# Performance work log

Measured on AMD Instinct MI355X. Metric: run time of the kernel, lower is better.

The kernel has to match this reference:

```python
import jax, jax.numpy as jnp
import numpy as np

MODES = (16, 16)
EMBED_DIM = 64
NUM_HEADS = 8


def spectral_conv(x, w):
    """FNO-style spectral conv. x: [B,S,Ci,H,W]; w: [Ci,Co,mx,my,2] (real/imag)."""
    wc = w[..., 0] + 1j * w[..., 1]
    H, W = x.shape[-2], x.shape[-1]
    mx, my = wc.shape[2], wc.shape[3]
    xf = jnp.fft.rfft2(x)                                   # [B,S,Ci,H,W//2+1]
    of = jnp.einsum('bsixy,ioxy->bsoxy', xf[..., :mx, :my], wc)
    out_f = jnp.zeros(x.shape[:2] + (wc.shape[1], H, W // 2 + 1), dtype=of.dtype)
    out_f = out_f.at[..., :mx, :my].set(of)
    return jnp.fft.irfft2(out_f, s=(H, W))


def log_cpb_bias(n_sub_x, n_sub_y, w1, b1, w2):
    """Swin-v2-style log-spaced continuous position bias -> [heads, S, S]."""
    cx = jnp.arange(n_sub_x, dtype=jnp.float32)
    cy = jnp.arange(n_sub_y, dtype=jnp.float32)
    coords = jnp.stack(jnp.meshgrid(cx, cy, indexing='ij'), axis=-1).reshape(-1, 2)
    rel = coords[:, None, :] - coords[None, :, :]           # [S,S,2]
    rel = jnp.sign(rel) * jnp.log1p(jnp.abs(rel))
    h = jax.nn.relu(rel @ w1 + b1)                          # [S,S,hidden]
    bias = h @ w2                                           # [S,S,heads]
    return jnp.transpose(bias, (2, 0, 1))


def _unflatten(f, num_heads, embed_dim):
    # [B,S,h*d,H,W] -> [B,h,S,d,H,W]
    B, S = f.shape[0], f.shape[1]
    f = f.reshape(B, S, num_heads, embed_dim, f.shape[-2], f.shape[-1])
    return jnp.transpose(f, (0, 2, 1, 3, 4, 5))


def setup_inputs() -> dict:
    key = jax.random.key(0)
    ks = jax.random.split(key, 9)
    B, S, D, H, W = 2, 64, EMBED_DIM, 32, 32
    hd = NUM_HEADS * D
    mx, my = MODES
    scale = 0.02
    return {
        'seq': jax.random.normal(ks[0], (B, S, D, H, W), dtype=jnp.float32),
        'wq': scale * jax.random.normal(ks[1], (D, hd, mx, my, 2), dtype=jnp.float32),
        'wk': scale * jax.random.normal(ks[2], (D, hd, mx, my, 2), dtype=jnp.float32),
        'wv': scale * jax.random.normal(ks[3], (D, hd, mx, my, 2), dtype=jnp.float32),
        'wo': scale * jax.random.normal(ks[4], (hd, D, mx, my, 2), dtype=jnp.float32),
        'cpb_w1': scale * jax.random.normal(ks[5], (2, D), dtype=jnp.float32),
        'cpb_b1': jnp.zeros((D,), dtype=jnp.float32),
        'cpb_w2': scale * jax.random.normal(ks[6], (D, NUM_HEADS), dtype=jnp.float32),
        'n_sub_x': 8,
        'n_sub_y': 8,
    }


def reference(seq, wq, wk, wv, wo, cpb_w1, cpb_b1, cpb_w2, n_sub_x, n_sub_y):
    q = _unflatten(spectral_conv(seq, wq), NUM_HEADS, EMBED_DIM)  # [B,h,S,d,H,W]
    k = _unflatten(spectral_conv(seq, wk), NUM_HEADS, EMBED_DIM)
    v = _unflatten(spectral_conv(seq, wv), NUM_HEADS, EMBED_DIM)

    bias = log_cpb_bias(n_sub_x, n_sub_y, cpb_w1, cpb_b1, cpb_w2)  # [h,S,S]

    d, H, W = q.shape[-3], q.shape[-2], q.shape[-1]
    scale = 1.0 / jnp.sqrt(jnp.asarray(d * H * W, dtype=q.dtype))
    scores = jnp.einsum('bhqdxy,bhkdxy->bhqk', q, k) * scale + bias[None]
    attn = jax.nn.softmax(scores, axis=-1)
    sa = jnp.einsum('bhqk,bhkdxy->bhqdxy', attn, v)          # [B,h,S,d,H,W]

    # _flatten: [B,h,S,d,H,W] -> [B,S,h*d,H,W]
    sa = jnp.transpose(sa, (0, 2, 1, 3, 4, 5))
    B, S = sa.shape[0], sa.shape[1]
    sa = sa.reshape(B, S, NUM_HEADS * EMBED_DIM, H, W)
    return spectral_conv(sa, wo)
```

## Files before the change

kernel.cpp:

```cpp
#include <hip/hip_runtime.h>

#define TWO_PI 6.28318530717958647692f

#define NH 8
#define CH 128
#define NCH 2

#define OFF_XM   0ull
#define OFF_WTA  (OFF_XM + 8388608ull)
#define OFF_WTB  (OFF_WTA + 16777216ull)
#define OFF_PO   (OFF_WTB + 16777216ull)
#define OFF_ATTN (OFF_PO + 16777216ull)
#define WS_TOTAL (OFF_ATTN + 262144ull)

typedef short bf16x8 __attribute__((ext_vector_type(8)));
typedef float f32x4 __attribute__((ext_vector_type(4)));
#define MFMA_B16(a, b, c) __builtin_amdgcn_mfma_f32_16x16x32_bf16(a, b, c, 0, 0, 0)

__device__ __forceinline__ float bl(unsigned u) { return __uint_as_float(u << 16); }
__device__ __forceinline__ unsigned short f2b(float f) {
    unsigned u = __float_as_uint(f);
    return (unsigned short)((u + 0x7fffu + ((u >> 16) & 1u)) >> 16);
}
__device__ __forceinline__ unsigned pack2(float lo, float hi) {
    return (unsigned)f2b(lo) | ((unsigned)f2b(hi) << 16);
}

__device__ __forceinline__ bf16x8 mkfrag(const unsigned* __restrict__ Wt, int co_l, int ri,
                                         int ci0, bool dc) {
    unsigned a0 = Wt[(ci0 + 0) * 64 + (co_l ^ (ci0 + 0))];
    unsigned a1 = Wt[(ci0 + 1) * 64 + (co_l ^ (ci0 + 1))];
    unsigned a2 = Wt[(ci0 + 2) * 64 + (co_l ^ (ci0 + 2))];
    unsigned a3 = Wt[(ci0 + 3) * 64 + (co_l ^ (ci0 + 3))];
    uint4 r;
    if (ri) {
        if (dc) { r.x = 0u; r.y = 0u; r.z = 0u; r.w = 0u; }
        else {
            r.x = (a0 >> 16) | (a0 << 16); r.y = (a1 >> 16) | (a1 << 16);
            r.z = (a2 >> 16) | (a2 << 16); r.w = (a3 >> 16) | (a3 << 16);
        }
    } else {
        r.x = a0 ^ 0x80000000u; r.y = a1 ^ 0x80000000u;
        r.z = a2 ^ 0x80000000u; r.w = a3 ^ 0x80000000u;
    }
    return __builtin_bit_cast(bf16x8, r);
}

__global__ __launch_bounds__(256) void k_transpose2(const float* __restrict__ srcA, unsigned* __restrict__ dstA, int kindA,
                                                    const float* __restrict__ srcB, unsigned* __restrict__ dstB, int kindB,
                                                    int m0) {
    const float* in = (blockIdx.z == 0) ? srcA : srcB;
    unsigned* outp = (blockIdx.z == 0) ? dstA : dstB;
    int kind = (blockIdx.z == 0) ? kindA : kindB;
    __shared__ unsigned T[16][65];
    int tid = threadIdx.x;
    int r0 = blockIdx.x * 64;
    int ci, h;
    if (kind == 2) { h = r0 >> 12; ci = (r0 >> 6) & 63; }
    else           { ci = r0 >> 9; h = (r0 >> 6) & 7; }
    int ml0 = blockIdx.y * 16;
    int u = (m0 + ml0) >> 4;
    const float2* in2 = (const float2*)in;
    #pragma unroll
    for (int p = 0; p < 4; ++p) {
        int f = tid + p * 256;
        int row = f >> 4, mc = f & 15;
        float fac = (kind == 0) ? (mc > 0 ? 1.41421356f : (u > 0 ? 0.70710678f : 1.f))
                  : (kind == 1) ? (mc > 0 ? 1.f : (u > 0 ? 0.5f : 1.f)) : 1.f;
        float2 v = in2[(size_t)(r0 + row) * 256 + m0 + ml0 + mc];
        T[mc][row] = pack2(v.x * fac, v.y * fac);
    }
    __syncthreads();
    #pragma unroll
    for (int p = 0; p < 4; ++p) {
        int f = tid + p * 256;
        int ml = f >> 6, co = f & 63;
        outp[((size_t)((ml0 + ml) * 8 + h) << 12) + ci * 64 + co] = T[ml][co];
    }
}

__global__ __launch_bounds__(256) void k_rfft(const float* __restrict__ seq,
                                              unsigned short* __restrict__ XM) {
    __shared__ float c32[32], s32[32];
    __shared__ float fld[32][33];
    __shared__ float tre[512], tim[512];
    __shared__ float obuf[256][18];
    int tid = threadIdx.x;
    int cig = blockIdx.x;
    int bs = blockIdx.y;
    if (tid < 32) { float s, c; __sincosf(TWO_PI * tid / 32.0f, &s, &c); c32[tid] = c; s32[tid] = s; }
    for (int cl = 0; cl < 8; ++cl) {
        int ci = cig * 8 + cl;
        const float2* src = (const float2*)(seq + ((size_t)bs * 64 + ci) * 1024);
        for (int p = 0; p < 2; ++p) {
            int idx2 = tid + p * 256;
            float2 v = src[idx2];
            int x = idx2 >> 4, y2 = (idx2 & 15) * 2;
            fld[x][y2] = v.x; fld[x][y2 + 1] = v.y;
        }
        __syncthreads();
        for (int p = 0; p < 2; ++p) {
            int e = tid + p * 256;
            int x = e >> 4, v = e & 15;
            float sr = 0.f, si = 0.f;
            for (int y = 0; y < 32; ++y) {
                float f = fld[x][y];
                int ph = (v * y) & 31;
                sr = fmaf(f, c32[ph], sr);
                si = fmaf(-f, s32[ph], si);
            }
            tre[x * 16 + v] = sr; tim[x * 16 + v] = si;
        }
        __syncthreads();
        {
            int u = tid >> 4, v = tid & 15;
            float xr = 0.f, xi = 0.f;
            for (int x = 0; x < 32; ++x) {
                float tr = tre[x * 16 + v], ti = tim[x * 16 + v];
                int ph = (u * x) & 31;
                float c = c32[ph], s = s32[ph];
                xr += tr * c + ti * s;
                xi += ti * c - tr * s;
            }
            obuf[tid][cl * 2] = xr; obuf[tid][cl * 2 + 1] = xi;
        }
        __syncthreads();
    }
    uint4 a, b;
    a.x = pack2(obuf[tid][0], obuf[tid][1]);
    a.y = pack2(obuf[tid][2], obuf[tid][3]);
    a.z = pack2(obuf[tid][4], obuf[tid][5]);
    a.w = pack2(obuf[tid][6], obuf[tid][7]);
    b.x = pack2(obuf[tid][8], obuf[tid][9]);
    b.y = pack2(obuf[tid][10], obuf[tid][11]);
    b.z = pack2(obuf[tid][12], obuf[tid][13]);
    b.w = pack2(obuf[tid][14], obuf[tid][15]);
    uint4* op = (uint4*)(XM + (((size_t)tid * 128 + bs) * 64 + cig * 8) * 2);
    op[0] = a; op[1] = b;
}

__global__ __launch_bounds__(512) void k_qks(const unsigned short* __restrict__ XM,
                                             const unsigned* __restrict__ WQ,
                                             const unsigned* __restrict__ WK,
                                             float* __restrict__ part, int mbase) {
    __shared__ __align__(16) unsigned char Xs[16384];
    __shared__ __align__(16) unsigned Wq[4096];
    __shared__ __align__(16) unsigned Wk[4096];
    __shared__ __align__(16) unsigned char Qs[16384];
    __shared__ __align__(16) unsigned char Ks[16384];
    int tid = threadIdx.x;
    int mg = blockIdx.x, h = blockIdx.y, b = blockIdx.z;
    int lane = tid & 63, w = tid >> 6;
    int lr = lane & 15, lg = lane >> 4;
    int wr = w & 1, wc = w >> 1;
    int sxa = (lr & 7) << 4;
    int ri = lr & 1;
    f32x4 zf = {0.f, 0.f, 0.f, 0.f};
    f32x4 sacc[2];
    sacc[0] = zf; sacc[1] = zf;
    for (int mm = 0; mm < 4; ++mm) {
        int ml = mg * 4 + mm;
        int mode = mbase + ml;
        bool dc = (mode == 0);
        __syncthreads();
        {
            const unsigned short* xg = XM + ((size_t)mode * 128 + b * 64) * 128;
            #pragma unroll
            for (int p = 0; p < 2; ++p) {
                int g = tid + p * 512; int row = g >> 4, c16 = g & 15;
                uint4 v = *(const uint4*)(xg + row * 128 + c16 * 8);
                *(uint4*)(Xs + row * 256 + ((c16 * 16) ^ ((row & 7) << 4))) = v;
            }
        }
        {
            const unsigned* tq = WQ + ((size_t)(ml * 8 + h) << 12);
            const unsigned* tk = WK + ((size_t)(ml * 8 + h) << 12);
            #pragma unroll
            for (int p = 0; p < 16; ++p) {
                int idx = tid + p * 512;
                int r = idx & 4095;
                int ci = r >> 6, co = r & 63;
                if (idx < 4096) Wq[ci * 64 + (co ^ ci)] = tq[r];
                else            Wk[ci * 64 + (co ^ ci)] = tk[r];
            }
        }
        __syncthreads();
        {
            f32x4 qa[2][2], ka[2][2];
            #pragma unroll
            for (int m = 0; m < 2; ++m)
                #pragma unroll
                for (int n = 0; n < 2; ++n) { qa[m][n] = zf; ka[m][n] = zf; }
            #pragma unroll
            for (int ks = 0; ks < 4; ++ks) {
                int kb = (ks * 64 + lg * 16) ^ sxa;
                int ci0 = ks * 16 + lg * 4;
                bf16x8 a0 = *(const bf16x8*)(Xs + (wr * 32 + lr) * 256 + kb);
                bf16x8 a1 = *(const bf16x8*)(Xs + (wr * 32 + 16 + lr) * 256 + kb);
                #pragma unroll
                for (int n = 0; n < 2; ++n) {
                    int co_l = wc * 16 + n * 8 + (lr >> 1);
                    bf16x8 bq = mkfrag(Wq, co_l, ri, ci0, dc);
                    bf16x8 bk = mkfrag(Wk, co_l, ri, ci0, dc);
                    qa[0][n] = MFMA_B16(a0, bq, qa[0][n]);
                    qa[1][n] = MFMA_B16(a1, bq, qa[1][n]);
                    ka[0][n] = MFMA_B16(a0, bk, ka[0][n]);
                    ka[1][n] = MFMA_B16(a1, bk, ka[1][n]);
                }
            }
            #pragma unroll
            for (int m = 0; m < 2; ++m)
                #pragma unroll
                for (int n = 0; n < 2; ++n) {
                    int colb = (wc * 32 + n * 16 + lr) * 2;
                    #pragma unroll
                    for (int r = 0; r < 4; ++r) {
                        int row = wr * 32 + m * 16 + lg * 4 + r;
                        int swz = (row & 7) << 4;
                        *(unsigned short*)(Qs + row * 256 + (colb ^ swz)) = f2b(qa[m][n][r]);
                        *(unsigned short*)(Ks + row * 256 + (colb ^ swz)) = f2b(ka[m][n][r]);
                    }
                }
        }
        __syncthreads();
        {
            #pragma unroll
            for (int ks = 0; ks < 4; ++ks) {
                int kb = (ks * 64 + lg * 16) ^ sxa;
                bf16x8 a0 = *(const bf16x8*)(Qs + (wr * 32 + lr) * 256 + kb);
                bf16x8 a1 = *(const bf16x8*)(Qs + (wr * 32 + 16 + lr) * 256 + kb);
                bf16x8 b0 = *(const bf16x8*)(Ks + (wc * 16 + lr) * 256 + kb);
                sacc[0] = MFMA_B16(a0, b0, sacc[0]);
                sacc[1] = MFMA_B16(a1, b0, sacc[1]);
            }
        }
    }
    float* pp = part + (((size_t)((mbase >> 2) + mg) * 16 + b * 8 + h) << 12);
    #pragma unroll
    for (int m = 0; m < 2; ++m)
        #pragma unroll
        for (int r = 0; r < 4; ++r)
            pp[(wr * 32 + m * 16 + lg * 4 + r) * 64 + wc * 16 + lr] = sacc[m][r];
}

__global__ void k_softmax(const float* __restrict__ part,
                          const float* __restrict__ w1, const float* __restrict__ b1,
                          const float* __restrict__ w2, unsigned short* __restrict__ attnb) {
    int j = threadIdx.x;
    int i = blockIdx.x;
    int bh = blockIdx.y;
    int h = bh & 7;
    float s = 0.f;
    for (int mg = 0; mg < 64; ++mg)
        s += part[(((size_t)mg * 16 + bh) * 64 + i) * 64 + j];
    float dx = (float)((i >> 3) - (j >> 3));
    float dy = (float)((i & 7) - (j & 7));
    float rx = (dx > 0.f ? 1.f : (dx < 0.f ? -1.f : 0.f)) * log1pf(fabsf(dx));
    float ry = (dy > 0.f ? 1.f : (dy < 0.f ? -1.f : 0.f)) * log1pf(fabsf(dy));
    float bias = 0.f;
    for (int l = 0; l < 64; ++l) {
        float hv = fmaxf(rx * w1[l] + ry * w1[64 + l] + b1[l], 0.f);
        bias = fmaf(hv, w2[l * NH + h], bias);
    }
    s = s * (1.0f / 262144.0f) + bias;
    float m = s;
    for (int o = 32; o >= 1; o >>= 1) m = fmaxf(m, __shfl_xor(m, o));
    float e = expf(s - m);
    float t = e;
    for (int o = 32; o >= 1; o >>= 1) t += __shfl_xor(t, o);
    attnb[((size_t)bh * 64 + i) * 64 + j] = f2b(e / t);
}

__global__ __launch_bounds__(512) void k_savo(const unsigned short* __restrict__ XM,
                                              const unsigned* __restrict__ WV,
                                              const unsigned* __restrict__ WO,
                                              const unsigned short* __restrict__ attnb,
                                              float* __restrict__ outf, int mbase) {
    __shared__ __align__(16) unsigned char Xs[16384];
    __shared__ __align__(16) unsigned Wv[4096];
    __shared__ __align__(16) unsigned Wo[4096];
    __shared__ __align__(16) unsigned char Vt[16384];
    __shared__ __align__(16) unsigned char Ss[16384];
    int tid = threadIdx.x;
    int ml = blockIdx.x, b = blockIdx.y;
    int mode = mbase + ml;
    bool dc = (mode == 0);
    int lane = tid & 63, w = tid >> 6;
    int lr = lane & 15, lg = lane >> 4;
    int wr = w & 1, wc = w >> 1;
    int sxa = (lr & 7) << 4;
    int ri = lr & 1;
    f32x4 zf = {0.f, 0.f, 0.f, 0.f};
    {
        const unsigned short* xg = XM + ((size_t)mode * 128 + b * 64) * 128;
        #pragma unroll
        for (int p = 0; p < 2; ++p) {
            int g = tid + p * 512; int row = g >> 4, c16 = g & 15;
            uint4 v = *(const uint4*)(xg + row * 128 + c16 * 8);
            *(uint4*)(Xs + row * 256 + ((c16 * 16) ^ ((row & 7) << 4))) = v;
        }
    }
    f32x4 oacc[2][2];
    oacc[0][0] = zf; oacc[0][1] = zf; oacc[1][0] = zf; oacc[1][1] = zf;
    for (int h = 0; h < NH; ++h) {
        __syncthreads();
        {
            const unsigned* tv = WV + ((size_t)(ml * 8 + h) << 12);
            const unsigned* to = WO + ((size_t)(ml * 8 + h) << 12);
            #pragma unroll
            for (int p = 0; p < 16; ++p) {
                int idx = tid + p * 512;
                int r = idx & 4095;
                int ci = r >> 6, co = r & 63;
                if (idx < 4096) Wv[ci * 64 + (co ^ ci)] = tv[r];
                else            Wo[ci * 64 + (co ^ ci)] = to[r];
            }
        }
        bf16x8 af[2][2];
        #pragma unroll
        for (int m = 0; m < 2; ++m)
            #pragma unroll
            for (int ks = 0; ks < 2; ++ks) {
                int irow = wr * 32 + m * 16 + lr;
                af[m][ks] = *(const bf16x8*)(attnb + (((size_t)(b * 8 + h) * 64 + irow) * 64 + ks * 32 + lg * 8));
            }
        __syncthreads();
        {
            f32x4 va[2][2];
            va[0][0] = zf; va[0][1] = zf; va[1][0] = zf; va[1][1] = zf;
            #pragma unroll
            for (int ks = 0; ks < 4; ++ks) {
                int kb = (ks * 64 + lg * 16) ^ sxa;
                int ci0 = ks * 16 + lg * 4;
                bf16x8 a0 = *(const bf16x8*)(Xs + (wr * 32 + lr) * 256 + kb);
                bf16x8 a1 = *(const bf16x8*)(Xs + (wr * 32 + 16 + lr) * 256 + kb);
                #pragma unroll
                for (int n = 0; n < 2; ++n) {
                    int co_l = wc * 16 + n * 8 + (lr >> 1);
                    bf16x8 bb = mkfrag(Wv, co_l, ri, ci0, dc);
                    va[0][n] = MFMA_B16(a0, bb, va[0][n]);
                    va[1][n] = MFMA_B16(a1, bb, va[1][n]);
                }
            }
            #pragma unroll
            for (int m = 0; m < 2; ++m)
                #pragma unroll
                for (int n = 0; n < 2; ++n) {
                    int cp = wc * 32 + n * 16 + lr;
                    int j0 = wr * 32 + m * 16 + lg * 4;
                    uint2 t;
                    t.x = pack2(va[m][n][0], va[m][n][1]);
                    t.y = pack2(va[m][n][2], va[m][n][3]);
                    *(uint2*)(Vt + cp * 128 + ((j0 * 2) ^ ((cp & 7) << 4))) = t;
                }
        }
        __syncthreads();
        {
            f32x4 sa_[2][2];
            sa_[0][0] = zf; sa_[0][1] = zf; sa_[1][0] = zf; sa_[1][1] = zf;
            #pragma unroll
            for (int ks = 0; ks < 2; ++ks) {
                #pragma unroll
                for (int n = 0; n < 2; ++n) {
                    int cp = wc * 32 + n * 16 + lr;
                    bf16x8 bb = *(const bf16x8*)(Vt + cp * 128 + ((ks * 64 + lg * 16) ^ ((cp & 7) << 4)));
                    sa_[0][n] = MFMA_B16(af[0][ks], bb, sa_[0][n]);
                    sa_[1][n] = MFMA_B16(af[1][ks], bb, sa_[1][n]);
                }
            }
            #pragma unroll
            for (int m = 0; m < 2; ++m)
                #pragma unroll
                for (int n = 0; n < 2; ++n) {
                    int colb = (wc * 32 + n * 16 + lr) * 2;
                    #pragma unroll
                    for (int r = 0; r < 4; ++r) {
                        int row = wr * 32 + m * 16 + lg * 4 + r;
                        *(unsigned short*)(Ss + row * 256 + (colb ^ ((row & 7) << 4))) = f2b(sa_[m][n][r]);
                    }
                }
        }
        __syncthreads();
        {
            #pragma unroll
            for (int ks = 0; ks < 4; ++ks) {
                int kb = (ks * 64 + lg * 16) ^ sxa;
                int ci0 = ks * 16 + lg * 4;
                bf16x8 a0 = *(const bf16x8*)(Ss + (wr * 32 + lr) * 256 + kb);
                bf16x8 a1 = *(const bf16x8*)(Ss + (wr * 32 + 16 + lr) * 256 + kb);
                #pragma unroll
                for (int n = 0; n < 2; ++n) {
                    int co_l = wc * 16 + n * 8 + (lr >> 1);
                    bf16x8 bb = mkfrag(Wo, co_l, ri, ci0, false);
                    oacc[0][n] = MFMA_B16(a0, bb, oacc[0][n]);
                    oacc[1][n] = MFMA_B16(a1, bb, oacc[1][n]);
                }
            }
        }
    }
    #pragma unroll
    for (int m = 0; m < 2; ++m)
        #pragma unroll
        for (int n = 0; n < 2; ++n)
            #pragma unroll
            for (int r = 0; r < 4; ++r) {
                int i = wr * 32 + m * 16 + lg * 4 + r;
                int c2p = wc * 32 + n * 16 + lr;
                outf[((size_t)mode * 128 + b * 64 + i) * 128 + c2p] = oacc[m][n][r];
            }
}

__global__ __launch_bounds__(256) void k_irfft(const float* __restrict__ outf,
                                               float* __restrict__ out) {
    __shared__ float c32[32], s32[32];
    __shared__ float mf[256][18];
    __shared__ float sr[16 * 33], si[16 * 33];
    int tid = threadIdx.x;
    int cg = blockIdx.x;
    int bs = blockIdx.y;
    if (tid < 32) { float s, c; __sincosf(TWO_PI * tid / 32.0f, &s, &c); c32[tid] = c; s32[tid] = s; }
    {
        const float4* gp = (const float4*)(outf + (((size_t)tid * 128 + bs) * 64 + cg * 8) * 2);
        for (int q = 0; q < 4; ++q) {
            float4 v = gp[q];
            mf[tid][q * 4 + 0] = v.x; mf[tid][q * 4 + 1] = v.y;
            mf[tid][q * 4 + 2] = v.z; mf[tid][q * 4 + 3] = v.w;
        }
    }
    __syncthreads();
    for (int cc = 0; cc < 8; ++cc) {
        for (int p = 0; p < 2; ++p) {
            int e = tid + p * 256;
            int u = e >> 5, y = e & 31;
            float fr0 = mf[u * 16][cc * 2];
            float fi0 = (u == 0) ? 0.f : mf[u * 16][cc * 2 + 1];
            float ssr = 0.5f * fr0, ssi = 0.5f * fi0;
            for (int v = 1; v < 16; ++v) {
                float fr = mf[u * 16 + v][cc * 2], fi = mf[u * 16 + v][cc * 2 + 1];
                int ph = (v * y) & 31;
                float c = c32[ph], s = s32[ph];
                ssr += fr * c - fi * s;
                ssi += fr * s + fi * c;
            }
            sr[u * 33 + y] = ssr; si[u * 33 + y] = ssi;
        }
        __syncthreads();
        float res[4];
        for (int p = 0; p < 4; ++p) {
            int pos = tid + p * 256;
            int x = pos >> 5, y = pos & 31;
            float acc = 0.f;
            for (int u = 0; u < 16; ++u) {
                int ph = (u * x) & 31;
                acc += sr[u * 33 + y] * c32[ph] - si[u * 33 + y] * s32[ph];
            }
            res[p] = acc * (1.0f / 512.0f);
        }
        float* op = out + ((size_t)(bs * 64 + cg * 8 + cc)) * 1024;
        for (int p = 0; p < 4; ++p) op[tid + p * 256] = res[p];
        __syncthreads();
    }
}

extern "C" void kernel_launch(void* const* d_in, const int* in_sizes, int n_in,
                              void* d_out, int out_size, void* d_ws, size_t ws_size,
                              hipStream_t stream) {
    (void)in_sizes; (void)n_in; (void)out_size;
    const float* seq = (const float*)d_in[0];
    const float* wq = (const float*)d_in[1];
    const float* wk = (const float*)d_in[2];
    const float* wv = (const float*)d_in[3];
    const float* wo = (const float*)d_in[4];
    const float* cw1 = (const float*)d_in[5];
    const float* cb1 = (const float*)d_in[6];
    const float* cw2 = (const float*)d_in[7];
    float* out = (float*)d_out;
    char* ws = (char*)d_ws;
    if (ws_size < WS_TOTAL) return;

    unsigned short* XM = (unsigned short*)(ws + OFF_XM);
    unsigned* WTA = (unsigned*)(ws + OFF_WTA);
    unsigned* WTB = (unsigned*)(ws + OFF_WTB);
    float* PART = (float*)(ws + OFF_PO);
    float* OUTF = (float*)(ws + OFF_PO);
    unsigned short* ATTNB = (unsigned short*)(ws + OFF_ATTN);

    k_rfft<<<dim3(8, 128), dim3(256), 0, stream>>>(seq, XM);

    for (int c = 0; c < NCH; ++c) {
        int m0 = c * CH;
        k_transpose2<<<dim3(512, CH / 16, 2), dim3(256), 0, stream>>>(wq, WTA, 0, wk, WTB, 0, m0);
        k_qks<<<dim3(CH / 4, NH, 2), dim3(512), 0, stream>>>(XM, WTA, WTB, PART, m0);
    }
    k_softmax<<<dim3(64, 16), dim3(64), 0, stream>>>(PART, cw1, cb1, cw2, ATTNB);

    for (int c = 0; c < NCH; ++c) {
        int m0 = c * CH;
        k_transpose2<<<dim3(512, CH / 16, 2), dim3(256), 0, stream>>>(wv, WTA, 1, wo, WTB, 2, m0);
        k_savo<<<dim3(CH, 2), dim3(512), 0, stream>>>(XM, WTA, WTB, ATTNB, OUTF, m0);
    }
    k_irfft<<<dim3(8, 128), dim3(256), 0, stream>>>(OUTF, out);
}
```

Baseline: 389.2 us.

## Split forward rFFT into separate y-pass and x-pass kernels via workspace buffer

```diff
diff --git a/kernel.cpp b/kernel.cpp
--- a/kernel.cpp
+++ b/kernel.cpp
@@ -79,63 +79,72 @@
     }
 }
 
-__global__ __launch_bounds__(256) void k_rfft(const float* __restrict__ seq,
-                                              unsigned short* __restrict__ XM) {
+__global__ __launch_bounds__(256) void k_rfft_y(const float* __restrict__ seq,
+                                                float2* __restrict__ T) {
     __shared__ float c32[32], s32[32];
     __shared__ float fld[32][33];
-    __shared__ float tre[512], tim[512];
-    __shared__ float obuf[256][18];
+    int tid = threadIdx.x;
+    int bc = blockIdx.x;
+    if (tid < 32) { float s, c; __sincosf(TWO_PI * tid / 32.0f, &s, &c); c32[tid] = c; s32[tid] = s; }
+    float4 v = ((const float4*)(seq + (size_t)bc * 1024))[tid];
+    int x = tid >> 3, y4 = (tid & 7) * 4;
+    fld[x][y4] = v.x; fld[x][y4 + 1] = v.y; fld[x][y4 + 2] = v.z; fld[x][y4 + 3] = v.w;
+    __syncthreads();
+    float2* op = T + (size_t)bc * 512;
+    #pragma unroll
+    for (int p = 0; p < 2; ++p) {
+        int e = tid + p * 256;
+        int xx = e >> 4, vv = e & 15;
+        float sr = 0.f, si = 0.f;
+        #pragma unroll
+        for (int y = 0; y < 32; ++y) {
+            float f = fld[xx][y];
+            int ph = (vv * y) & 31;
+            sr = fmaf(f, c32[ph], sr);
+            si = fmaf(-f, s32[ph], si);
+        }
+        float2 t; t.x = sr; t.y = si;
+        op[e] = t;
+    }
+}
+
+__global__ __launch_bounds__(256) void k_rfft_x(const float2* __restrict__ T,
+                                                unsigned short* __restrict__ XM) {
+    __shared__ float c32[32], s32[32];
+    __shared__ float2 t[8][512];
     int tid = threadIdx.x;
     int cig = blockIdx.x;
     int bs = blockIdx.y;
     if (tid < 32) { float s, c; __sincosf(TWO_PI * tid / 32.0f, &s, &c); c32[tid] = c; s32[tid] = s; }
-    for (int cl = 0; cl < 8; ++cl) {
-        int ci = cig * 8 + cl;
-        const float2* src = (const float2*)(seq + ((size_t)bs * 64 + ci) * 1024);
-        for (int p = 0; p < 2; ++p) {
-            int idx2 = tid + p * 256;
-            float2 v = src[idx2];
-            int x = idx2 >> 4, y2 = (idx2 & 15) * 2;
-            fld[x][y2] = v.x; fld[x][y2 + 1] = v.y;
-        }
-        __syncthreads();
-        for (int p = 0; p < 2; ++p) {
-            int e = tid + p * 256;
-            int x = e >> 4, v = e & 15;
-            float sr = 0.f, si = 0.f;
-            for (int y = 0; y < 32; ++y) {
-                float f = fld[x][y];
-                int ph = (v * y) & 31;
-                sr = fmaf(f, c32[ph], sr);
-                si = fmaf(-f, s32[ph], si);
-            }
-            tre[x * 16 + v] = sr; tim[x * 16 + v] = si;
-        }
-        __syncthreads();
-        {
-            int u = tid >> 4, v = tid & 15;
-            float xr = 0.f, xi = 0.f;
-            for (int x = 0; x < 32; ++x) {
-                float tr = tre[x * 16 + v], ti = tim[x * 16 + v];
-                int ph = (u * x) & 31;
-                float c = c32[ph], s = s32[ph];
-                xr += tr * c + ti * s;
-                xi += ti * c - tr * s;
-            }
-            obuf[tid][cl * 2] = xr; obuf[tid][cl * 2 + 1] = xi;
-        }
-        __syncthreads();
-    }
+    const float4* src = (const float4*)(T + ((size_t)bs * 64 + cig * 8) * 512);
+    #pragma unroll
+    for (int p = 0; p < 8; ++p) {
+        int idx = tid + p * 256;
+        float4 w = src[idx];
+        int ch = idx >> 8, r2 = idx & 255;
+        float2 t0; t0.x = w.x; t0.y = w.y;
+        float2 t1; t1.x = w.z; t1.y = w.w;
+        t[ch][r2 * 2] = t0; t[ch][r2 * 2 + 1] = t1;
+    }
+    __syncthreads();
+    int u = tid >> 4, vv = tid & 15;
+    unsigned outw[8];
+    for (int ch = 0; ch < 8; ++ch) {
+        float xr = 0.f, xi = 0.f;
+        #pragma unroll
+        for (int x = 0; x < 32; ++x) {
+            float2 tv = t[ch][x * 16 + vv];
+            int ph = (u * x) & 31;
+            float c = c32[ph], s = s32[ph];
+            xr += tv.x * c + tv.y * s;
+            xi += tv.y * c - tv.x * s;
+        }
+        outw[ch] = pack2(xr, xi);
+    }
+    uint4* op = (uint4*)(XM + (((size_t)tid * 128 + bs) * 64 + cig * 8) * 2);
     uint4 a, b;
-    a.x = pack2(obuf[tid][0], obuf[tid][1]);
-    a.y = pack2(obuf[tid][2], obuf[tid][3]);
-    a.z = pack2(obuf[tid][4], obuf[tid][5]);
-    a.w = pack2(obuf[tid][6], obuf[tid][7]);
-    b.x = pack2(obuf[tid][8], obuf[tid][9]);
-    b.y = pack2(obuf[tid][10], obuf[tid][11]);
-    b.z = pack2(obuf[tid][12], obuf[tid][13]);
-    b.w = pack2(obuf[tid][14], obuf[tid][15]);
-    uint4* op = (uint4*)(XM + (((size_t)tid * 128 + bs) * 64 + cig * 8) * 2);
+    a.x = outw[0]; a.y = outw[1]; a.z = outw[2]; a.w = outw[3];
+    b.x = outw[4]; b.y = outw[5]; b.z = outw[6]; b.w = outw[7];
     op[0] = a; op[1] = b;
 }
 
@@ -481,11 +490,13 @@
     unsigned short* XM = (unsigned short*)(ws + OFF_XM);
     unsigned* WTA = (unsigned*)(ws + OFF_WTA);
     unsigned* WTB = (unsigned*)(ws + OFF_WTB);
+    float2* Tbuf = (float2*)(ws + OFF_WTA);
     float* PART = (float*)(ws + OFF_PO);
     float* OUTF = (float*)(ws + OFF_PO);
     unsigned short* ATTNB = (unsigned short*)(ws + OFF_ATTN);
 
-    k_rfft<<<dim3(8, 128), dim3(256), 0, stream>>>(seq, XM);
+    k_rfft_y<<<dim3(8192), dim3(256), 0, stream>>>(seq, Tbuf);
+    k_rfft_x<<<dim3(8, 128), dim3(256), 0, stream>>>(Tbuf, XM);
 
     for (int c = 0; c < NCH; ++c) {
         int m0 = c * CH;
```

Result: faster. 353.9 us (-9.1%).
